# Kernel optimization log

Hardware: AMD Instinct MI355X
Metric: run time of the kernel (lower is better)

The kernel has to match this reference:

```python
import jax, jax.numpy as jnp
import numpy as np

KS = 5
STRIDE = 1


def extract_patches(x, ks, s):
    # TF tf.image.extract_patches ordering: (row, col, channel) flattened
    B, H, W, C = x.shape
    oh = (H - ks) // s + 1
    ow = (W - ks) // s + 1
    cols = [x[:, i:i + (oh - 1) * s + 1:s, j:j + (ow - 1) * s + 1:s, :]
            for i in range(ks) for j in range(ks)]
    p = jnp.stack(cols, axis=3)  # [B, oh, ow, ks*ks, C]
    return p.reshape(B, oh * ow, ks * ks * C)


def setup_inputs() -> dict:
    key = jax.random.key(0)
    k1, k2, k3 = jax.random.split(key, 3)
    B, H, W, C, K = 32, 14, 14, 32, 64
    mu_in = jax.random.normal(k1, (B, H, W, C), dtype=jnp.float32)
    Sigma_in = jax.random.uniform(k2, (B, H * W, H * W, C), dtype=jnp.float32)
    w_mu = 0.05 * jax.random.normal(k3, (KS, KS, C, K), dtype=jnp.float32)
    w_sigma = jnp.full((K,), -2.2, dtype=jnp.float32)
    return {"mu_in": mu_in, "Sigma_in": Sigma_in, "w_mu": w_mu, "w_sigma": w_sigma}


def reference(mu_in, Sigma_in, w_mu, w_sigma):
    B, H, W, C = mu_in.shape
    ks = w_mu.shape[0]
    K = w_mu.shape[-1]
    s = STRIDE

    # mean path: standard conv2d, NHWC / HWIO
    mu_out = jax.lax.conv_general_dilated(
        mu_in, w_mu, (s, s), 'VALID',
        dimension_numbers=('NHWC', 'HWIO', 'NHWC'))

    # diag of Sigma_in over the two N dims: [B,N,N,C] -> [B,C,N] -> [B,H,W,C]
    diag_sigma = jnp.diagonal(Sigma_in, axis1=1, axis2=2)           # [B,C,N]
    diag_sigma = jnp.transpose(diag_sigma, (0, 2, 1)).reshape(B, H, W, C)

    dsg = extract_patches(diag_sigma, ks, s)                        # [B,P,M]
    P = dsg.shape[1]

    mu_cov_sq = (w_mu * w_mu).reshape(-1, K)                        # [M,K]
    v1 = dsg @ mu_cov_sq                                            # [B,P,K]

    sp = jnp.log1p(jnp.exp(w_sigma))                                # softplus, [K]
    tr = jnp.sum(dsg, axis=2, keepdims=True)                        # [B,P,1]
    diag_vals = v1 + sp[None, None, :] * tr                         # [B,P,K] (trace1 + mu_wT_sigmags_mu_w diags)

    mu_p = extract_patches(mu_in, ks, s)                            # [B,P,M]
    G = jnp.einsum('bpm,bqm->bpq', mu_p, mu_p)                      # [B,P,P]

    Sigma_out = sp[None, None, None, :] * G[..., None]              # [B,P,P,K]
    ip = jnp.arange(P)
    Sigma_out = Sigma_out.at[:, ip, ip, :].add(diag_vals)

    Sigma_out = jnp.where(jnp.isnan(Sigma_out), 0.0, Sigma_out)
    Sigma_out = jnp.where(jnp.isinf(Sigma_out), 0.0, Sigma_out)

    # TF set_diag acts on the LAST two dims ([P,K] inner matrices) -- reproduce exactly
    m = min(P, K)
    ii = jnp.arange(m)
    Sigma_out = Sigma_out.at[:, :, ii, ii].set(jnp.abs(Sigma_out[:, :, ii, ii]))
    return mu_out, Sigma_out
```

## Files before the change

kernel.cpp:

```cpp
#include <hip/hip_runtime.h>
#include <cmath>

typedef __attribute__((ext_vector_type(8))) short short8;
typedef __attribute__((ext_vector_type(4))) float f32x4;

#define NB 32
#define MU_OUT_SZ (NB*100*64)
#define LDAP 56

#define WS_WF 0
#define WS_G  204800
#define WS_DV 1484800

__device__ inline unsigned short f2bf(float f) {
  unsigned u = __builtin_bit_cast(unsigned, f);
  u += 0x7fffu + ((u >> 16) & 1u);
  return (unsigned short)(u >> 16);
}

__global__ __launch_bounds__(256) void prepW(
    const float* __restrict__ w_mu, const float* __restrict__ w_sigma,
    unsigned short* __restrict__ wf) {
  __shared__ float wsh[2048];
  const int ij = blockIdx.x, t = threadIdx.x;
  const float4* src = (const float4*)(w_mu + (size_t)ij * 2048);
  ((float4*)wsh)[t]       = src[t];
  ((float4*)wsh)[t + 256] = src[t + 256];
  __syncthreads();
#pragma unroll
  for (int id0 = 0; id0 < 512; id0 += 256) {
    const int id = id0 + t;
    const int kind = id >> 8;
    const int rest = id & 255;
    const int n = rest >> 6, l = rest & 63;
    const int col = n * 16 + (l & 15);
    const int m0 = (l >> 4) * 8;
    const float sp = log1pf(expf(w_sigma[col]));
    unsigned short v[8];
#pragma unroll
    for (int i = 0; i < 8; ++i) {
      const float wv = wsh[(m0 + i) * 64 + col];
      const float x = kind ? (wv * wv + sp) : wv;
      v[i] = f2bf(x);
    }
    uint4 pk;
    pk.x = v[0] | ((unsigned)v[1] << 16);
    pk.y = v[2] | ((unsigned)v[3] << 16);
    pk.z = v[4] | ((unsigned)v[5] << 16);
    pk.w = v[6] | ((unsigned)v[7] << 16);
    *(uint4*)(wf + (size_t)((ij * 8 + kind * 4 + n) * 64 + l) * 8) = pk;
  }
}

__global__ __launch_bounds__(512) void gemm(
    const float* __restrict__ mu_in, const float* __restrict__ Sigma_in,
    const unsigned short* __restrict__ wf,
    float* __restrict__ G, float* __restrict__ dv, float* __restrict__ out) {
  __shared__ unsigned short mu_sh[196 * LDAP];
  __shared__ unsigned short sd_sh[196 * LDAP];
  const int r = blockIdx.x;
  const int b = blockIdx.y;
  const int t = threadIdx.x, l = t & 63, w = t >> 6;

  const float4* mu4 = (const float4*)(mu_in + (size_t)b * 6272);
  for (int f = t; f < 1568; f += 512) {
    const float4 v = mu4[f];
    const int row = f >> 3, c = (f & 7) * 4;
    ushort4 pv;
    pv.x = f2bf(v.x); pv.y = f2bf(v.y); pv.z = f2bf(v.z); pv.w = f2bf(v.w);
    *(ushort4*)(mu_sh + row * LDAP + c) = pv;
    const float4 s = *(const float4*)(Sigma_in +
        ((size_t)(b * 196 + row) * 196 + row) * 32 + c);
    ushort4 ps;
    ps.x = f2bf(s.x); ps.y = f2bf(s.y); ps.z = f2bf(s.z); ps.w = f2bf(s.w);
    *(ushort4*)(sd_sh + row * LDAP + c) = ps;
  }
  __syncthreads();

  const int laneP = l & 15, g16 = (l >> 4) * 8;
  const int pA = (r * 16 + laneP > 99) ? 99 : r * 16 + laneP;
  const int baseA = ((pA / 10) * 14 + (pA % 10)) * LDAP + g16;
  const bool doG = (w < 7);
  const int q = w * 16 + laneP;
  const int qc = q > 99 ? 99 : q;
  const int baseB = ((qc / 10) * 14 + (qc % 10)) * LDAP + g16;
  const bool doMu = (w < 4);
  const int n = doMu ? w : (w - 4);
  const int kslot = doMu ? n : (4 + n);

  const short8* wfp = (const short8*)wf;
  short8 fw = wfp[(size_t)kslot * 64 + l];
  f32x4 aG = {}, aX = {};
  for (int ij = 0; ij < 25; ++ij) {
    const short8 fw_n = (ij < 24) ? wfp[(size_t)((ij + 1) * 8 + kslot) * 64 + l] : fw;
    const int off = ((ij / 5) * 14 + (ij % 5)) * LDAP;
    if (doG) {
      const short8 fA = *(const short8*)(mu_sh + baseA + off);
      const short8 fB = *(const short8*)(mu_sh + baseB + off);
      aG = __builtin_amdgcn_mfma_f32_16x16x32_bf16(fA, fB, aG, 0, 0, 0);
      if (doMu) {
        aX = __builtin_amdgcn_mfma_f32_16x16x32_bf16(fA, fw, aX, 0, 0, 0);
      } else {
        const short8 fS = *(const short8*)(sd_sh + baseA + off);
        aX = __builtin_amdgcn_mfma_f32_16x16x32_bf16(fS, fw, aX, 0, 0, 0);
      }
    } else {
      const short8 fS = *(const short8*)(sd_sh + baseA + off);
      aX = __builtin_amdgcn_mfma_f32_16x16x32_bf16(fS, fw, aX, 0, 0, 0);
    }
    fw = fw_n;
  }

  const int prow0 = (l >> 4) * 4;
  if (doG && q < 100) {
    float* Gb = G + (size_t)b * 10000;
#pragma unroll
    for (int j = 0; j < 4; ++j) {
      const int row = r * 16 + prow0 + j;
      if (row < 100) Gb[row * 100 + q] = aG[j];
    }
  }
  const int k = n * 16 + laneP;
  if (doMu) {
    float* mo = out + (size_t)b * 6400;
#pragma unroll
    for (int j = 0; j < 4; ++j) {
      const int p = r * 16 + prow0 + j;
      if (p < 100) mo[p * 64 + k] = aX[j];
    }
  } else {
    float* dvb = dv + (size_t)b * 6400;
#pragma unroll
    for (int j = 0; j < 4; ++j) {
      const int p = r * 16 + prow0 + j;
      if (p < 100) dvb[p * 64 + k] = aX[j];
    }
  }
}

__global__ __launch_bounds__(256) void writer(
    const float* __restrict__ G, const float* __restrict__ dv,
    const float* __restrict__ w_sigma, float* __restrict__ out) {
  const unsigned tid = blockIdx.x * 256 + threadIdx.x;
  const int k4 = (tid & 15) * 4;
  const float4 wsv = *(const float4*)(w_sigma + k4);
  f32x4 sp4;
  sp4.x = log1pf(expf(wsv.x));
  sp4.y = log1pf(expf(wsv.y));
  sp4.z = log1pf(expf(wsv.z));
  sp4.w = log1pf(expf(wsv.w));
  float* sig = out + MU_OUT_SZ;
  for (unsigned l4 = tid; l4 < 5120000u; l4 += 524288u) {
    const unsigned rr = l4 >> 4;
    const unsigned q = rr % 100u;
    const unsigned pq = rr / 100u;
    const unsigned p = pq % 100u;
    const float g = G[rr];
    f32x4 v;
    v.x = sp4.x * g; v.y = sp4.y * g; v.z = sp4.z * g; v.w = sp4.w * g;
    if (q == p) {
      const float4 dvv = *(const float4*)(dv + (size_t)pq * 64 + k4);
      v.x += dvv.x; v.y += dvv.y; v.z += dvv.z; v.w += dvv.w;
    }
    v.x = (q == (unsigned)k4)     ? fabsf(v.x) : v.x;
    v.y = (q == (unsigned)k4 + 1) ? fabsf(v.y) : v.y;
    v.z = (q == (unsigned)k4 + 2) ? fabsf(v.z) : v.z;
    v.w = (q == (unsigned)k4 + 3) ? fabsf(v.w) : v.w;
    __builtin_nontemporal_store(v, (f32x4*)(sig + (size_t)l4 * 4));
  }
}

extern "C" void kernel_launch(void* const* d_in, const int* in_sizes, int n_in,
                              void* d_out, int out_size, void* d_ws, size_t ws_size,
                              hipStream_t stream) {
  const float* mu_in    = (const float*)d_in[0];
  const float* Sigma_in = (const float*)d_in[1];
  const float* w_mu     = (const float*)d_in[2];
  const float* w_sigma  = (const float*)d_in[3];
  float* out = (float*)d_out;
  unsigned char* ws = (unsigned char*)d_ws;
  unsigned short* wf = (unsigned short*)(ws + WS_WF);
  float* G  = (float*)(ws + WS_G);
  float* dv = (float*)(ws + WS_DV);

  prepW<<<25, 256, 0, stream>>>(w_mu, w_sigma, wf);
  gemm<<<dim3(7, NB), 512, 0, stream>>>(mu_in, Sigma_in, wf, G, dv, out);
  writer<<<2048, 256, 0, stream>>>(G, dv, w_sigma, out);
}
```

Measured before the change: 33.42 us.

## Fuse Sigma_out writer into the GEMM kernel using shared-memory G and dv

The separate writer kernel is merged into the GEMM kernel. Each block keeps its 16-row tile of G and the diagonal values in shared memory and writes its own slice of Sigma_out straight from there. This removes the global-memory round trip for G and dv and one kernel launch. In exchange, the large output write is now issued by only 224 blocks of 512 threads, which may reduce memory-level parallelism for the dominant store traffic.

```diff
diff --git a/kernel.cpp b/kernel.cpp
--- a/kernel.cpp
+++ b/kernel.cpp
@@ -7,10 +7,6 @@
 #define NB 32
 #define MU_OUT_SZ (NB*100*64)
 #define LDAP 56
-
-#define WS_WF 0
-#define WS_G  204800
-#define WS_DV 1484800
 
 __device__ inline unsigned short f2bf(float f) {
   unsigned u = __builtin_bit_cast(unsigned, f);
@@ -52,12 +48,14 @@
   }
 }
 
-__global__ __launch_bounds__(512) void gemm(
+__global__ __launch_bounds__(512) void fusedK(
     const float* __restrict__ mu_in, const float* __restrict__ Sigma_in,
-    const unsigned short* __restrict__ wf,
-    float* __restrict__ G, float* __restrict__ dv, float* __restrict__ out) {
+    const unsigned short* __restrict__ wf, const float* __restrict__ w_sigma,
+    float* __restrict__ out) {
   __shared__ unsigned short mu_sh[196 * LDAP];
   __shared__ unsigned short sd_sh[196 * LDAP];
+  __shared__ float g_sh[16][100];
+  __shared__ float dv_sh[16][64];
   const int r = blockIdx.x;
   const int b = blockIdx.y;
   const int t = threadIdx.x, l = t & 63, w = t >> 6;
@@ -113,12 +111,8 @@
 
   const int prow0 = (l >> 4) * 4;
   if (doG && q < 100) {
-    float* Gb = G + (size_t)b * 10000;
 #pragma unroll
-    for (int j = 0; j < 4; ++j) {
-      const int row = r * 16 + prow0 + j;
-      if (row < 100) Gb[row * 100 + q] = aG[j];
-    }
+    for (int j = 0; j < 4; ++j) g_sh[prow0 + j][q] = aG[j];
   }
   const int k = n * 16 + laneP;
   if (doMu) {
@@ -129,43 +123,37 @@
       if (p < 100) mo[p * 64 + k] = aX[j];
     }
   } else {
-    float* dvb = dv + (size_t)b * 6400;
 #pragma unroll
-    for (int j = 0; j < 4; ++j) {
-      const int p = r * 16 + prow0 + j;
-      if (p < 100) dvb[p * 64 + k] = aX[j];
-    }
+    for (int j = 0; j < 4; ++j) dv_sh[prow0 + j][k] = aX[j];
   }
-}
+  __syncthreads();
 
-__global__ __launch_bounds__(256) void writer(
-    const float* __restrict__ G, const float* __restrict__ dv,
-    const float* __restrict__ w_sigma, float* __restrict__ out) {
-  const unsigned tid = blockIdx.x * 256 + threadIdx.x;
-  const int k4 = (tid & 15) * 4;
+  const int nrows = (r == 6) ? 4 : 16;
+  const int p0 = r * 16;
+  const int k4 = (t & 15) * 4;
   const float4 wsv = *(const float4*)(w_sigma + k4);
   f32x4 sp4;
   sp4.x = log1pf(expf(wsv.x));
   sp4.y = log1pf(expf(wsv.y));
   sp4.z = log1pf(expf(wsv.z));
   sp4.w = log1pf(expf(wsv.w));
-  float* sig = out + MU_OUT_SZ;
-  for (unsigned l4 = tid; l4 < 5120000u; l4 += 524288u) {
-    const unsigned rr = l4 >> 4;
-    const unsigned q = rr % 100u;
-    const unsigned pq = rr / 100u;
-    const unsigned p = pq % 100u;
-    const float g = G[rr];
+  float* sig = out + MU_OUT_SZ + ((size_t)(b * 100 + p0) * 100) * 64;
+  const int total = nrows * 1600;
+  for (int l4 = t; l4 < total; l4 += 512) {
+    const int row = l4 / 1600;
+    const int rem = l4 - row * 1600;
+    const int qq = rem >> 4;
+    const float g = g_sh[row][qq];
     f32x4 v;
     v.x = sp4.x * g; v.y = sp4.y * g; v.z = sp4.z * g; v.w = sp4.w * g;
-    if (q == p) {
-      const float4 dvv = *(const float4*)(dv + (size_t)pq * 64 + k4);
+    if (qq == p0 + row) {
+      const float4 dvv = *(const float4*)&dv_sh[row][k4];
       v.x += dvv.x; v.y += dvv.y; v.z += dvv.z; v.w += dvv.w;
     }
-    v.x = (q == (unsigned)k4)     ? fabsf(v.x) : v.x;
-    v.y = (q == (unsigned)k4 + 1) ? fabsf(v.y) : v.y;
-    v.z = (q == (unsigned)k4 + 2) ? fabsf(v.z) : v.z;
-    v.w = (q == (unsigned)k4 + 3) ? fabsf(v.w) : v.w;
+    v.x = (qq == k4)     ? fabsf(v.x) : v.x;
+    v.y = (qq == k4 + 1) ? fabsf(v.y) : v.y;
+    v.z = (qq == k4 + 2) ? fabsf(v.z) : v.z;
+    v.w = (qq == k4 + 3) ? fabsf(v.w) : v.w;
     __builtin_nontemporal_store(v, (f32x4*)(sig + (size_t)l4 * 4));
   }
 }
@@ -178,12 +166,8 @@
   const float* w_mu     = (const float*)d_in[2];
   const float* w_sigma  = (const float*)d_in[3];
   float* out = (float*)d_out;
-  unsigned char* ws = (unsigned char*)d_ws;
-  unsigned short* wf = (unsigned short*)(ws + WS_WF);
-  float* G  = (float*)(ws + WS_G);
-  float* dv = (float*)(ws + WS_DV);
+  unsigned short* wf = (unsigned short*)d_ws;
 
   prepW<<<25, 256, 0, stream>>>(w_mu, w_sigma, wf);
-  gemm<<<dim3(7, NB), 512, 0, stream>>>(mu_in, Sigma_in, wf, G, dv, out);
-  writer<<<2048, 256, 0, stream>>>(G, dv, w_sigma, out);
+  fusedK<<<dim3(7, NB), 512, 0, stream>>>(mu_in, Sigma_in, wf, w_sigma, out);
 }
```

New measurement: 33.13 us. About the same (-0.9%).
